# Optimization experiments

Hardware: AMD Instinct MI355X
Metric: run time of the kernel (lower is better)

## Reference

```python
import jax, jax.numpy as jnp
import numpy as np


def setup_inputs() -> dict:
    key = jax.random.key(0)
    ks = jax.random.split(key, 8)
    bs, slen, d = 16, 2048, 1024
    scale = 1.0 / np.sqrt(d)
    return {
        "query": jax.random.normal(ks[0], (bs, d), jnp.float32),
        "states": jax.random.normal(ks[1], (bs, slen, d), jnp.float32),
        "Wq": jax.random.normal(ks[2], (d, d), jnp.float32) * scale,
        "bq": jax.random.normal(ks[3], (d,), jnp.float32) * 0.01,
        "Wk": jax.random.normal(ks[4], (d, d), jnp.float32) * scale,
        "bk": jax.random.normal(ks[5], (d,), jnp.float32) * 0.01,
        "We": jax.random.normal(ks[6], (2 * d,), jnp.float32) * scale,
        "be": jax.random.normal(ks[7], (1,), jnp.float32) * 0.01,
    }


def reference(query, states, Wq, bq, Wk, bk, We, be):
    d = Wq.shape[1]
    # q: (bs, d); k: (bs, slen, d)
    q = jax.nn.relu(query @ Wq + bq)
    k = jax.nn.relu(jnp.einsum("bsv,vd->bsd", states, Wk) + bk)
    # tanh(cat(q, k)) @ We == tanh(q) @ We[:d] + tanh(k) @ We[d:]
    # (avoids materializing the repeated/concatenated (bs, slen, 2d) tensor)
    We_q, We_k = We[:d], We[d:]
    energy = (jnp.tanh(q) @ We_q)[:, None] + jnp.einsum("bsd,d->bs", jnp.tanh(k), We_k) + be[0]
    attn_weights = jax.nn.softmax(energy, axis=1)  # (bs, slen)
    attn = jnp.einsum("bs,bsd->bd", attn_weights, states)  # weighted sum of values
    return attn_weights, attn
```

## Files before the change

kernel.cpp:

```cpp
#include <hip/hip_runtime.h>
#include <hip/hip_bf16.h>

#define D 1024
#define SLEN 2048
#define BS 16
#define MROWS (BS*SLEN)
#define NCHUNK (MROWS/64)

typedef __attribute__((ext_vector_type(8))) short short8;
typedef __attribute__((ext_vector_type(4))) float f32x4;

__device__ __forceinline__ short f2bf(float f) {
  __hip_bfloat16 h = __float2bfloat16(f);
  return __builtin_bit_cast(short, h);
}

__device__ __forceinline__ float4 ntload4(const float* p) {
  f32x4 v = __builtin_nontemporal_load((const f32x4*)p);
  float4 r; r.x = v.x; r.y = v.y; r.z = v.z; r.w = v.w; return r;
}

__global__ __launch_bounds__(256) void wk_prep(const float* __restrict__ Wk,
                                               short* __restrict__ WkT) {
  const int g = blockIdx.x;
  const int t = threadIdx.x;
#pragma unroll
  for (int it = 0; it < 4; ++it) {
    const int n = it*256 + t;
    short8 p;
#pragma unroll
    for (int j = 0; j < 8; ++j)
      p[j] = f2bf(Wk[(size_t)(g*8 + j)*D + n]);
    *(short8*)(WkT + ((size_t)g*D + n)*8) = p;
  }
}

__global__ __launch_bounds__(512, 2) void energy_gemm(
    const float* __restrict__ states, const short* __restrict__ WkT,
    const float* __restrict__ bk, const float* __restrict__ We,
    float* __restrict__ eraw, float* __restrict__ pattn,
    float* __restrict__ cmax, float* __restrict__ csum)
{
  __shared__ short Al[64 * 129 * 8];
  __shared__ float red2[64 * 8];
  __shared__ float pfin[64];

  const int tid  = threadIdx.x;
  const int w    = tid >> 6;
  const int lane = tid & 63;
  const int quad = lane >> 4;
  const int l16  = lane & 15;
  const int g    = blockIdx.x;
  const int m0   = g * 64;

  {
    const int row = tid >> 3;
    const int u0  = tid & 7;
    const float* Ag = states + (size_t)(m0 + row)*D;
#pragma unroll
    for (int i = 0; i < 16; ++i) {
      const int u = u0 + i*8;
      float4 x0 = ntload4(Ag + u*8);
      float4 x1 = ntload4(Ag + u*8 + 4);
      short8 p;
      p[0]=f2bf(x0.x); p[1]=f2bf(x0.y); p[2]=f2bf(x0.z); p[3]=f2bf(x0.w);
      p[4]=f2bf(x1.x); p[5]=f2bf(x1.y); p[6]=f2bf(x1.z); p[7]=f2bf(x1.w);
      *(short8*)(Al + ((size_t)row*129 + u)*8) = p;
    }
  }
  __syncthreads();

  f32x4 acc[2][4][4];
#pragma unroll
  for (int nc = 0; nc < 2; ++nc)
#pragma unroll
    for (int mi = 0; mi < 4; ++mi)
#pragma unroll
      for (int ni = 0; ni < 4; ++ni)
        acc[nc][mi][ni] = (f32x4){0.f, 0.f, 0.f, 0.f};

  const short* bbase = WkT + ((size_t)quad*D + w*128 + l16)*8;
  const short* abase = Al + ((size_t)l16*129 + quad)*8;

#define LOADB(ks, buf)                                                   \
  {                                                                      \
    const short* bp = bbase + (size_t)(ks)*32768;                        \
    _Pragma("unroll")                                                    \
    for (int nc = 0; nc < 2; ++nc)                                       \
      _Pragma("unroll")                                                  \
      for (int ni = 0; ni < 4; ++ni)                                     \
        buf[nc*4 + ni] = *(const short8*)(bp + nc*512 + ni*128);         \
  }

#define LOADA(ks, buf)                                                   \
  {                                                                      \
    _Pragma("unroll")                                                    \
    for (int mi = 0; mi < 4; ++mi)                                       \
      buf[mi] = *(const short8*)(abase + mi*16512 + (ks)*32);            \
  }

#define MFMAS(fa, fb)                                                    \
  {                                                                      \
    _Pragma("unroll")                                                    \
    for (int nc = 0; nc < 2; ++nc)                                       \
      _Pragma("unroll")                                                  \
      for (int mi = 0; mi < 4; ++mi)                                     \
        _Pragma("unroll")                                                \
        for (int ni = 0; ni < 4; ++ni)                                   \
          acc[nc][mi][ni] = __builtin_amdgcn_mfma_f32_16x16x32_bf16(     \
              fa[mi], fb[nc*4 + ni], acc[nc][mi][ni], 0, 0, 0);          \
  }

  short8 fa0[4], fa1[4], fb0[8], fb1[8];
  LOADA(0, fa0); LOADB(0, fb0);
#pragma unroll
  for (int kk = 0; kk < 16; ++kk) {
    LOADA(2*kk + 1, fa1); LOADB(2*kk + 1, fb1);
    MFMAS(fa0, fb0);
    if (kk < 15) { LOADA(2*kk + 2, fa0); LOADB(2*kk + 2, fb0); }
    MFMAS(fa1, fb1);
  }

  float esum[16];
#pragma unroll
  for (int q = 0; q < 16; ++q) esum[q] = 0.f;
#pragma unroll
  for (int nc = 0; nc < 2; ++nc)
#pragma unroll
    for (int ni = 0; ni < 4; ++ni) {
      const int n = w*128 + nc*64 + ni*16 + l16;
      const float bkv = bk[n];
      const float wev = We[D + n];
#pragma unroll
      for (int mi = 0; mi < 4; ++mi)
#pragma unroll
        for (int r = 0; r < 4; ++r) {
          float x = acc[nc][mi][ni][r] + bkv;
          x = fmaxf(x, 0.f);
          float ex = __expf(2.f * x);
          float th = 1.f - 2.f/(ex + 1.f);
          esum[mi*4 + r] += th * wev;
        }
    }
#pragma unroll
  for (int dd = 1; dd < 16; dd <<= 1)
#pragma unroll
    for (int q = 0; q < 16; ++q)
      esum[q] += __shfl_xor(esum[q], dd, 64);

  if (l16 == 0) {
#pragma unroll
    for (int mi = 0; mi < 4; ++mi)
#pragma unroll
      for (int r = 0; r < 4; ++r)
        red2[(mi*16 + quad*4 + r)*8 + w] = esum[mi*4 + r];
  }
  __syncthreads();

  if (tid < 64) {
    float e = 0.f;
#pragma unroll
    for (int wi = 0; wi < 8; ++wi) e += red2[tid*8 + wi];
    eraw[m0 + tid] = e;
    float mm = e;
#pragma unroll
    for (int dd = 1; dd < 64; dd <<= 1) mm = fmaxf(mm, __shfl_xor(mm, dd, 64));
    const float pv = __expf(e - mm);
    float ss = pv;
#pragma unroll
    for (int dd = 1; dd < 64; dd <<= 1) ss += __shfl_xor(ss, dd, 64);
    pfin[tid] = pv;
    if (tid == 0) { cmax[g] = mm; csum[g] = ss; }
  }
  __syncthreads();

  {
    const int u    = tid >> 2;
    const int joff = (tid & 3) * 2;
    const short* ap = Al + (size_t)u*8 + joff;
    float a0 = 0.f, a1 = 0.f;
#pragma unroll 16
    for (int row = 0; row < 64; ++row) {
      const unsigned int bits = *(const unsigned int*)(ap + (size_t)row*1032);
      const float pv = pfin[row];
      const float lo = __builtin_bit_cast(float, bits << 16);
      const float hi = __builtin_bit_cast(float, bits & 0xffff0000u);
      a0 = fmaf(pv, lo, a0);
      a1 = fmaf(pv, hi, a1);
    }
    float2 o; o.x = a0; o.y = a1;
    *(float2*)(pattn + (size_t)g*D + 2*tid) = o;
  }
#undef LOADB
#undef LOADA
#undef MFMAS
}

__global__ __launch_bounds__(256) void attn_finalize(
    const float* __restrict__ eraw, const float* __restrict__ pattn,
    const float* __restrict__ cmax, const float* __restrict__ csum,
    float* __restrict__ wts, float* __restrict__ attn)
{
  const int b = blockIdx.x;
  const int t = threadIdx.x;
  __shared__ float scl[32];
  __shared__ float stats[2];

  if (t < 32) {
    const float m = cmax[b*32 + t];
    float mm = m;
#pragma unroll
    for (int dd = 1; dd < 32; dd <<= 1) mm = fmaxf(mm, __shfl_xor(mm, dd, 64));
    const float e = __expf(m - mm);
    scl[t] = e;
    float s = e * csum[b*32 + t];
#pragma unroll
    for (int dd = 1; dd < 32; dd <<= 1) s += __shfl_xor(s, dd, 64);
    if (t == 0) { stats[0] = mm; stats[1] = 1.f / s; }
  }
  __syncthreads();
  const float m_b = stats[0];
  const float inv = stats[1];

#pragma unroll
  for (int j = 0; j < 8; ++j) {
    const int s = j*256 + t;
    wts[(size_t)b*SLEN + s] = __expf(eraw[(size_t)b*SLEN + s] - m_b) * inv;
  }

  float acc[4] = {0.f, 0.f, 0.f, 0.f};
#pragma unroll
  for (int c = 0; c < 32; ++c) {
    const float sc = scl[c];
    const float* pp = pattn + ((size_t)(b*32 + c))*D + t;
#pragma unroll
    for (int j = 0; j < 4; ++j)
      acc[j] = fmaf(sc, pp[j*256], acc[j]);
  }
#pragma unroll
  for (int j = 0; j < 4; ++j)
    attn[(size_t)b*D + j*256 + t] = acc[j] * inv;
}

extern "C" void kernel_launch(void* const* d_in, const int* in_sizes, int n_in,
                              void* d_out, int out_size, void* d_ws, size_t ws_size,
                              hipStream_t stream) {
  const float* states = (const float*)d_in[1];
  const float* Wk     = (const float*)d_in[4];
  const float* bk     = (const float*)d_in[5];
  const float* We     = (const float*)d_in[6];
  float* out = (float*)d_out;

  char* ws = (char*)d_ws;
  short* WkT   = (short*)ws;                                  ws += (size_t)D*D*sizeof(short);
  float* eraw  = (float*)ws;                                  ws += (size_t)MROWS*sizeof(float);
  float* pattn = (float*)ws;                                  ws += (size_t)NCHUNK*D*sizeof(float);
  float* cmaxp = (float*)ws;                                  ws += (size_t)NCHUNK*sizeof(float);
  float* csump = (float*)ws;

  (void)in_sizes; (void)n_in; (void)out_size; (void)ws_size;

  wk_prep<<<128, 256, 0, stream>>>(Wk, WkT);
  energy_gemm<<<NCHUNK, 512, 0, stream>>>(states, WkT, bk, We, eraw, pattn, cmaxp, csump);
  attn_finalize<<<BS, 256, 0, stream>>>(eraw, pattn, cmaxp, csump, out, out + MROWS);
}
```

Baseline: 274.2 us.

## Halve row chunk to 32 rows and raise occupancy to four blocks per CU

Each energy_gemm block now handles 32 rows of states instead of 64, which halves LDS use and the accumulator registers. Launch bounds go from 2 to 4 blocks per CU, and the explicit double-buffered register prefetch is replaced by a simple unroll-2 k-loop. The intent is to hide latency through occupancy rather than software pipelining. In exchange, every WkT tile is re-read twice as often per row, and finalize has to reduce 64 chunks per batch instead of 32.

```diff
diff --git a/kernel.cpp b/kernel.cpp
--- a/kernel.cpp
+++ b/kernel.cpp
@@ -5,7 +5,9 @@
 #define SLEN 2048
 #define BS 16
 #define MROWS (BS*SLEN)
-#define NCHUNK (MROWS/64)
+#define CROWS 32
+#define NCHUNK (MROWS/CROWS)
+#define CPB (SLEN/CROWS)
 
 typedef __attribute__((ext_vector_type(8))) short short8;
 typedef __attribute__((ext_vector_type(4))) float f32x4;
@@ -35,15 +37,15 @@
   }
 }
 
-__global__ __launch_bounds__(512, 2) void energy_gemm(
+__global__ __launch_bounds__(512, 4) void energy_gemm(
     const float* __restrict__ states, const short* __restrict__ WkT,
     const float* __restrict__ bk, const float* __restrict__ We,
     float* __restrict__ eraw, float* __restrict__ pattn,
     float* __restrict__ cmax, float* __restrict__ csum)
 {
-  __shared__ short Al[64 * 129 * 8];
-  __shared__ float red2[64 * 8];
-  __shared__ float pfin[64];
+  __shared__ short Al[CROWS * 129 * 8];
+  __shared__ float red2[CROWS * 8];
+  __shared__ float pfin[CROWS];
 
   const int tid  = threadIdx.x;
   const int w    = tid >> 6;
@@ -51,15 +53,15 @@
   const int quad = lane >> 4;
   const int l16  = lane & 15;
   const int g    = blockIdx.x;
-  const int m0   = g * 64;
+  const int m0   = g * CROWS;
 
   {
-    const int row = tid >> 3;
-    const int u0  = tid & 7;
+    const int row = tid >> 4;
+    const int u0  = tid & 15;
     const float* Ag = states + (size_t)(m0 + row)*D;
 #pragma unroll
-    for (int i = 0; i < 16; ++i) {
-      const int u = u0 + i*8;
+    for (int i = 0; i < 8; ++i) {
+      const int u = u0 + i*16;
       float4 x0 = ntload4(Ag + u*8);
       float4 x1 = ntload4(Ag + u*8 + 4);
       short8 p;
@@ -70,11 +72,11 @@
   }
   __syncthreads();
 
-  f32x4 acc[2][4][4];
+  f32x4 acc[2][2][4];
 #pragma unroll
   for (int nc = 0; nc < 2; ++nc)
 #pragma unroll
-    for (int mi = 0; mi < 4; ++mi)
+    for (int mi = 0; mi < 2; ++mi)
 #pragma unroll
       for (int ni = 0; ni < 4; ++ni)
         acc[nc][mi][ni] = (f32x4){0.f, 0.f, 0.f, 0.f};
@@ -82,48 +84,30 @@
   const short* bbase = WkT + ((size_t)quad*D + w*128 + l16)*8;
   const short* abase = Al + ((size_t)l16*129 + quad)*8;
 
-#define LOADB(ks, buf)                                                   \
-  {                                                                      \
-    const short* bp = bbase + (size_t)(ks)*32768;                        \
-    _Pragma("unroll")                                                    \
-    for (int nc = 0; nc < 2; ++nc)                                       \
-      _Pragma("unroll")                                                  \
-      for (int ni = 0; ni < 4; ++ni)                                     \
-        buf[nc*4 + ni] = *(const short8*)(bp + nc*512 + ni*128);         \
-  }
-
-#define LOADA(ks, buf)                                                   \
-  {                                                                      \
-    _Pragma("unroll")                                                    \
-    for (int mi = 0; mi < 4; ++mi)                                       \
-      buf[mi] = *(const short8*)(abase + mi*16512 + (ks)*32);            \
-  }
-
-#define MFMAS(fa, fb)                                                    \
-  {                                                                      \
-    _Pragma("unroll")                                                    \
-    for (int nc = 0; nc < 2; ++nc)                                       \
-      _Pragma("unroll")                                                  \
-      for (int mi = 0; mi < 4; ++mi)                                     \
-        _Pragma("unroll")                                                \
-        for (int ni = 0; ni < 4; ++ni)                                   \
-          acc[nc][mi][ni] = __builtin_amdgcn_mfma_f32_16x16x32_bf16(     \
-              fa[mi], fb[nc*4 + ni], acc[nc][mi][ni], 0, 0, 0);          \
-  }
-
-  short8 fa0[4], fa1[4], fb0[8], fb1[8];
-  LOADA(0, fa0); LOADB(0, fb0);
-#pragma unroll
-  for (int kk = 0; kk < 16; ++kk) {
-    LOADA(2*kk + 1, fa1); LOADB(2*kk + 1, fb1);
-    MFMAS(fa0, fb0);
-    if (kk < 15) { LOADA(2*kk + 2, fa0); LOADB(2*kk + 2, fb0); }
-    MFMAS(fa1, fb1);
-  }
-
-  float esum[16];
-#pragma unroll
-  for (int q = 0; q < 16; ++q) esum[q] = 0.f;
+#pragma unroll 2
+  for (int ks = 0; ks < 32; ++ks) {
+    short8 fa[2], fbx[4];
+#pragma unroll
+    for (int mi = 0; mi < 2; ++mi)
+      fa[mi] = *(const short8*)(abase + mi*16512 + ks*32);
+    const short* bp = bbase + (size_t)ks*32768;
+#pragma unroll
+    for (int nc = 0; nc < 2; ++nc) {
+#pragma unroll
+      for (int ni = 0; ni < 4; ++ni)
+        fbx[ni] = *(const short8*)(bp + nc*512 + ni*128);
+#pragma unroll
+      for (int mi = 0; mi < 2; ++mi)
+#pragma unroll
+        for (int ni = 0; ni < 4; ++ni)
+          acc[nc][mi][ni] = __builtin_amdgcn_mfma_f32_16x16x32_bf16(
+              fa[mi], fbx[ni], acc[nc][mi][ni], 0, 0, 0);
+    }
+  }
+
+  float esum[8];
+#pragma unroll
+  for (int q = 0; q < 8; ++q) esum[q] = 0.f;
 #pragma unroll
   for (int nc = 0; nc < 2; ++nc)
 #pragma unroll
@@ -132,7 +116,7 @@
       const float bkv = bk[n];
       const float wev = We[D + n];
 #pragma unroll
-      for (int mi = 0; mi < 4; ++mi)
+      for (int mi = 0; mi < 2; ++mi)
 #pragma unroll
         for (int r = 0; r < 4; ++r) {
           float x = acc[nc][mi][ni][r] + bkv;
@@ -145,30 +129,30 @@
 #pragma unroll
   for (int dd = 1; dd < 16; dd <<= 1)
 #pragma unroll
-    for (int q = 0; q < 16; ++q)
+    for (int q = 0; q < 8; ++q)
       esum[q] += __shfl_xor(esum[q], dd, 64);
 
   if (l16 == 0) {
 #pragma unroll
-    for (int mi = 0; mi < 4; ++mi)
+    for (int mi = 0; mi < 2; ++mi)
 #pragma unroll
       for (int r = 0; r < 4; ++r)
         red2[(mi*16 + quad*4 + r)*8 + w] = esum[mi*4 + r];
   }
   __syncthreads();
 
-  if (tid < 64) {
+  if (tid < CROWS) {
     float e = 0.f;
 #pragma unroll
     for (int wi = 0; wi < 8; ++wi) e += red2[tid*8 + wi];
     eraw[m0 + tid] = e;
     float mm = e;
 #pragma unroll
-    for (int dd = 1; dd < 64; dd <<= 1) mm = fmaxf(mm, __shfl_xor(mm, dd, 64));
+    for (int dd = 1; dd < 32; dd <<= 1) mm = fmaxf(mm, __shfl_xor(mm, dd, 64));
     const float pv = __expf(e - mm);
     float ss = pv;
 #pragma unroll
-    for (int dd = 1; dd < 64; dd <<= 1) ss += __shfl_xor(ss, dd, 64);
+    for (int dd = 1; dd < 32; dd <<= 1) ss += __shfl_xor(ss, dd, 64);
     pfin[tid] = pv;
     if (tid == 0) { cmax[g] = mm; csum[g] = ss; }
   }
@@ -180,7 +164,7 @@
     const short* ap = Al + (size_t)u*8 + joff;
     float a0 = 0.f, a1 = 0.f;
 #pragma unroll 16
-    for (int row = 0; row < 64; ++row) {
+    for (int row = 0; row < CROWS; ++row) {
       const unsigned int bits = *(const unsigned int*)(ap + (size_t)row*1032);
       const float pv = pfin[row];
       const float lo = __builtin_bit_cast(float, bits << 16);
@@ -191,9 +175,6 @@
     float2 o; o.x = a0; o.y = a1;
     *(float2*)(pattn + (size_t)g*D + 2*tid) = o;
   }
-#undef LOADB
-#undef LOADA
-#undef MFMAS
 }
 
 __global__ __launch_bounds__(256) void attn_finalize(
@@ -203,19 +184,19 @@
 {
   const int b = blockIdx.x;
   const int t = threadIdx.x;
-  __shared__ float scl[32];
+  __shared__ float scl[CPB];
   __shared__ float stats[2];
 
-  if (t < 32) {
-    const float m = cmax[b*32 + t];
+  if (t < CPB) {
+    const float m = cmax[b*CPB + t];
     float mm = m;
 #pragma unroll
-    for (int dd = 1; dd < 32; dd <<= 1) mm = fmaxf(mm, __shfl_xor(mm, dd, 64));
+    for (int dd = 1; dd < 64; dd <<= 1) mm = fmaxf(mm, __shfl_xor(mm, dd, 64));
     const float e = __expf(m - mm);
     scl[t] = e;
-    float s = e * csum[b*32 + t];
-#pragma unroll
-    for (int dd = 1; dd < 32; dd <<= 1) s += __shfl_xor(s, dd, 64);
+    float s = e * csum[b*CPB + t];
+#pragma unroll
+    for (int dd = 1; dd < 64; dd <<= 1) s += __shfl_xor(s, dd, 64);
     if (t == 0) { stats[0] = mm; stats[1] = 1.f / s; }
   }
   __syncthreads();
@@ -230,9 +211,9 @@
 
   float acc[4] = {0.f, 0.f, 0.f, 0.f};
 #pragma unroll
-  for (int c = 0; c < 32; ++c) {
+  for (int c = 0; c < CPB; ++c) {
     const float sc = scl[c];
-    const float* pp = pattn + ((size_t)(b*32 + c))*D + t;
+    const float* pp = pattn + ((size_t)(b*CPB + c))*D + t;
 #pragma unroll
     for (int j = 0; j < 4; ++j)
       acc[j] = fmaf(sc, pp[j*256], acc[j]);
@@ -252,10 +233,10 @@
   float* out = (float*)d_out;
 
   char* ws = (char*)d_ws;
-  short* WkT   = (short*)ws;                                  ws += (size_t)D*D*sizeof(short);
-  float* eraw  = (float*)ws;                                  ws += (size_t)MROWS*sizeof(float);
-  float* pattn = (float*)ws;                                  ws += (size_t)NCHUNK*D*sizeof(float);
-  float* cmaxp = (float*)ws;                                  ws += (size_t)NCHUNK*sizeof(float);
+  short* WkT   = (short*)ws;  ws += (size_t)D*D*sizeof(short);
+  float* eraw  = (float*)ws;  ws += (size_t)MROWS*sizeof(float);
+  float* pattn = (float*)ws;  ws += (size_t)NCHUNK*D*sizeof(float);
+  float* cmaxp = (float*)ws;  ws += (size_t)NCHUNK*sizeof(float);
   float* csump = (float*)ws;
 
   (void)in_sizes; (void)n_in; (void)out_size; (void)ws_size;
```

New measurement: 287.2 us. +4.7%, slower.
